# Kernel tuning notes

Hardware: AMD Instinct MI355X
Metric: run time of the kernel (lower is better)

The kernel has to match this reference:

```python
import jax, jax.numpy as jnp
import numpy as np

N_NODES = 50000
N_EDGES = 800000
N_GRAPHS = 64
EPS = 1e-5


def glorot(key, shape):
    fan_in, fan_out = shape[0], shape[1]
    lim = np.sqrt(6.0 / (fan_in + fan_out))
    return jax.random.uniform(key, shape, jnp.float32, -lim, lim)


def setup_inputs() -> dict:
    key = jax.random.key(0)
    ks = jax.random.split(key, 12)
    x = jax.random.normal(ks[0], (N_NODES, 1), jnp.float32)
    edge_index = jax.random.randint(ks[1], (2, N_EDGES), 0, N_NODES, jnp.int64)
    batch = jnp.sort(jax.random.randint(ks[2], (N_NODES,), 0, N_GRAPHS, jnp.int64))
    dims = [(1, 256), (256, 256), (256, 128)]
    params = {}
    for i, (di, do) in enumerate(dims):
        params[f"Wl{i}"] = glorot(ks[3 + 3 * i], (di, do))          # neighbor (lin_l) weight
        params[f"b{i}"] = jnp.zeros((do,), jnp.float32)              # lin_l bias
        params[f"Wr{i}"] = glorot(ks[4 + 3 * i], (di, do))           # root (lin_r) weight
    params["gamma"] = jnp.ones((128,), jnp.float32)
    params["beta"] = jnp.zeros((128,), jnp.float32)
    return {"x": x, "edge_index": edge_index, "batch": batch, **params}


def _sage_conv(x, src, dst, deg_inv, Wl, b, Wr):
    # mean-aggregate messages x[src] at dst, then lin_l(agg) + lin_r(x)
    agg = jax.ops.segment_sum(x[src], dst, num_segments=N_NODES) * deg_inv
    return agg @ Wl + b + x @ Wr


def reference(x, edge_index, batch, Wl0, b0, Wr0, Wl1, b1, Wr1, Wl2, b2, Wr2, gamma, beta):
    src, dst = edge_index[0], edge_index[1]
    deg = jax.ops.segment_sum(jnp.ones((N_EDGES,), x.dtype), dst, num_segments=N_NODES)
    deg_inv = (1.0 / jnp.maximum(deg, 1.0))[:, None]

    h = _sage_conv(x, src, dst, deg_inv, Wl0, b0, Wr0)
    h = jax.nn.relu(h)  # dropout is identity in eval mode
    h = _sage_conv(h, src, dst, deg_inv, Wl1, b1, Wr1)
    h = jax.nn.relu(h)
    h = _sage_conv(h, src, dst, deg_inv, Wl2, b2, Wr2)

    # global mean pool over graphs
    gsum = jax.ops.segment_sum(h, batch, num_segments=N_GRAPHS)
    gcnt = jax.ops.segment_sum(jnp.ones((N_NODES,), h.dtype), batch, num_segments=N_GRAPHS)
    g = gsum / jnp.maximum(gcnt, 1.0)[:, None]

    # LayerNorm over feature dim
    mu = jnp.mean(g, axis=-1, keepdims=True)
    var = jnp.var(g, axis=-1, keepdims=True)
    return (g - mu) * jax.lax.rsqrt(var + EPS) * gamma + beta
```

## Files before the change

kernel.cpp:

```cpp
#include <hip/hip_runtime.h>
#include <stdint.h>

#define NN 50000
#define NE 800000
#define NG 64
#define F1 256
#define NNP 50176
#define NBK 196
#define NBS 392
#define EPB 2048
#define SCB 391
#define PCHUNKS 112
#define PKC 448

typedef __bf16 bf16x8 __attribute__((ext_vector_type(8)));
typedef float f32x4 __attribute__((ext_vector_type(4)));

__device__ __forceinline__ float bf2f(unsigned int u) {
  union { float f; unsigned int i; } v; v.i = (u & 0xffffu) << 16; return v.f;
}
__device__ __forceinline__ unsigned short f2bf(float f) {
  union { float f; unsigned int i; } v; v.f = f;
  unsigned int r = v.i + 0x7fffu + ((v.i >> 16) & 1u);
  return (unsigned short)(r >> 16);
}
__device__ __forceinline__ float asf(unsigned int u) {
  union { unsigned int u; float f; } v; v.u = u; return v.f;
}
__device__ __forceinline__ unsigned int asu(float f) {
  union { float f; unsigned int u; } v; v.f = f; return v.u;
}

__global__ void k_bhist(const int* __restrict__ ei, int* __restrict__ btot_d,
                        int* __restrict__ btot_s) {
  __shared__ int lhd[NBK];
  __shared__ int lhs[NBS];
  for (int i = threadIdx.x; i < NBK; i += 256) lhd[i] = 0;
  for (int i = threadIdx.x; i < NBS; i += 256) lhs[i] = 0;
  __syncthreads();
  for (int e = blockIdx.x * blockDim.x + threadIdx.x; e < NE; e += gridDim.x * blockDim.x) {
    atomicAdd(&lhs[ei[e] >> 7], 1);
    atomicAdd(&lhd[ei[NE + e] >> 8], 1);
  }
  __syncthreads();
  for (int i = threadIdx.x; i < NBK; i += 256) atomicAdd(&btot_d[i], lhd[i]);
  for (int i = threadIdx.x; i < NBS; i += 256) atomicAdd(&btot_s[i], lhs[i]);
}

__global__ void k_bscan(const int* __restrict__ btot_d, const int* __restrict__ btot_s,
                        int* __restrict__ bbase, int* __restrict__ bcur,
                        int* __restrict__ sbase, int* __restrict__ scur,
                        int* __restrict__ rowp) {
  __shared__ int buf[512];
  int t = threadIdx.x;
  int v = (t < NBK) ? btot_d[t] : 0;
  buf[t] = v;
  __syncthreads();
  for (int off = 1; off < 512; off <<= 1) {
    int o = (t >= off) ? buf[t - off] : 0;
    __syncthreads();
    buf[t] += o;
    __syncthreads();
  }
  if (t < NBK) { bbase[t] = buf[t] - v; bcur[t] = buf[t] - v; }
  if (t == NBK - 1) bbase[NBK] = buf[t];
  __syncthreads();
  int v2 = (t < NBS) ? btot_s[t] : 0;
  buf[t] = v2;
  __syncthreads();
  for (int off = 1; off < 512; off <<= 1) {
    int o = (t >= off) ? buf[t - off] : 0;
    __syncthreads();
    buf[t] += o;
    __syncthreads();
  }
  if (t < NBS) { sbase[t] = buf[t] - v2; scur[t] = buf[t] - v2; }
  if (t == NBS - 1) sbase[NBS] = buf[t];
  if (t == 0) rowp[NN] = NE;
}

__global__ __launch_bounds__(256) void k_bscatter(
    const int* __restrict__ ei, const float* __restrict__ x,
    int* __restrict__ bcur, int* __restrict__ scur,
    uint2* __restrict__ recs, unsigned int* __restrict__ srecs) {
  __shared__ int lhd[NBK]; __shared__ int gbd[NBK];
  __shared__ int lhs[NBS]; __shared__ int gbs[NBS];
  int b = blockIdx.x, tid = threadIdx.x;
  int e0 = b * EPB;
  for (int i = tid; i < NBK; i += 256) lhd[i] = 0;
  for (int i = tid; i < NBS; i += 256) lhs[i] = 0;
  __syncthreads();
  unsigned int meta[8]; float xv[8]; int lofd[8]; int bkd[8]; int lofs[8]; int bks[8];
#pragma unroll
  for (int i = 0; i < 8; ++i) {
    int e = e0 + i * 256 + tid;
    bkd[i] = -1;
    if (e < NE) {
      int s = ei[e], d = ei[NE + e];
      bkd[i] = d >> 8; bks[i] = s >> 7;
      meta[i] = (unsigned int)s | ((unsigned int)d << 16);
      xv[i] = x[s];
      lofd[i] = atomicAdd(&lhd[bkd[i]], 1);
      lofs[i] = atomicAdd(&lhs[bks[i]], 1);
    }
  }
  __syncthreads();
  for (int i = tid; i < NBK; i += 256) gbd[i] = atomicAdd(&bcur[i], lhd[i]);
  for (int i = tid; i < NBS; i += 256) gbs[i] = atomicAdd(&scur[i], lhs[i]);
  __syncthreads();
#pragma unroll
  for (int i = 0; i < 8; ++i) {
    if (bkd[i] >= 0) {
      recs[gbd[bkd[i]] + lofd[i]] = make_uint2(meta[i], asu(xv[i]));
      unsigned int s = meta[i] & 0xFFFFu, d = meta[i] >> 16;
      srecs[gbs[bks[i]] + lofs[i]] = d | ((s & 127u) << 16);
    }
  }
}

__global__ __launch_bounds__(256) void k_csr(
    const uint2* __restrict__ recs, const int* __restrict__ bbase,
    const float* __restrict__ x, const int* __restrict__ batch,
    int* __restrict__ rowp, float2* __restrict__ ax,
    int* __restrict__ colx, uint2* __restrict__ dg) {
  __shared__ int cnt[256];
  __shared__ int sc[256];
  __shared__ float xs[256];
  int b = blockIdx.x, tid = threadIdx.x;
  int eb = bbase[b], ee = bbase[b + 1];
  cnt[tid] = 0;
  xs[tid] = 0.0f;
  __syncthreads();
  for (int e = eb + tid; e < ee; e += 256) {
    uint2 r = recs[e];
    int dl = (r.x >> 16) & 255;
    atomicAdd(&cnt[dl], 1);
    atomicAdd(&xs[dl], asf(r.y));
  }
  __syncthreads();
  sc[tid] = cnt[tid];
  __syncthreads();
  for (int off = 1; off < 256; off <<= 1) {
    int o = (tid >= off) ? sc[tid - off] : 0;
    __syncthreads();
    sc[tid] += o;
    __syncthreads();
  }
  int excl = sc[tid] - cnt[tid];
  int i = b * 256 + tid;
  float dinv = 1.0f / fmaxf((float)cnt[tid], 1.0f);
  if (i < NN) {
    rowp[i] = eb + excl;
    ax[i] = make_float2(xs[tid] * dinv, x[i]);
    dg[i] = make_uint2(asu(dinv), (unsigned int)batch[i]);
  }
  __syncthreads();
  sc[tid] = excl;
  __syncthreads();
  for (int e = eb + tid; e < ee; e += 256) {
    uint2 r = recs[e];
    int dl = (r.x >> 16) & 255;
    int s = r.x & 0xFFFF;
    int slot = atomicAdd(&sc[dl], 1);
    colx[eb + slot] = s;
  }
}

__global__ __launch_bounds__(256) void k_csc(
    const unsigned int* __restrict__ srecs, const int* __restrict__ sbase,
    const uint2* __restrict__ dg, unsigned int* __restrict__ wgT2u) {
  __shared__ float wgrow[128 * 65];
  int b = blockIdx.x, tid = threadIdx.x;
  for (int i = tid; i < 128 * 65; i += 256) wgrow[i] = 0.0f;
  __syncthreads();
  int eb = sbase[b], ee = sbase[b + 1];
  for (int e = eb + tid; e < ee; e += 256) {
    unsigned int r = srecs[e];
    int d = r & 0xFFFF;
    int sl = (r >> 16) & 127;
    uint2 t = dg[d];
    atomicAdd(&wgrow[sl * 65 + t.y], asf(t.x));
  }
  __syncthreads();
  int s0u = b * 64;
  int k = tid & 63;
  for (int rr = 0; rr < 16; ++rr) {
    int g = rr * 4 + (tid >> 6);
    float w0 = wgrow[(2 * k) * 65 + g];
    float w1 = wgrow[(2 * k + 1) * 65 + g];
    unsigned short h0 = f2bf(w0), h1v = f2bf(w1);
    unsigned short l0 = f2bf(w0 - bf2f(h0)), l1 = f2bf(w1 - bf2f(h1v));
    wgT2u[(size_t)g * (NNP / 2) + s0u + k] = (unsigned int)h0 | ((unsigned int)h1v << 16);
    wgT2u[(size_t)(64 + g) * (NNP / 2) + s0u + k] = (unsigned int)l0 | ((unsigned int)l1 << 16);
  }
}

__global__ void k_cnt(const int* __restrict__ batch, int* __restrict__ cnt) {
  int g = threadIdx.x;
  if (g >= NG) return;
  int lo = 0, hi = NN;
  while (lo < hi) { int m = (lo + hi) >> 1; if (batch[m] < g) lo = m + 1; else hi = m; }
  int a = lo;
  lo = 0; hi = NN;
  while (lo < hi) { int m = (lo + hi) >> 1; if (batch[m] < g + 1) lo = m + 1; else hi = m; }
  cnt[g] = lo - a;
}

__global__ void k_axe(const int* __restrict__ colx, const float2* __restrict__ ax,
                      float2* __restrict__ axe) {
  int e = blockIdx.x * blockDim.x + threadIdx.x;
  if (e >= NE) return;
  axe[e] = ax[colx[e]];
}

__global__ void k_wprep(const float* __restrict__ Wl1, const float* __restrict__ Wr1,
                        unsigned short* __restrict__ wcat) {
  int t = blockIdx.x * blockDim.x + threadIdx.x;
  if (t >= 256 * 512) return;
  int n = t >> 9, k = t & 511;
  float v = (k < 256) ? Wl1[k * 256 + n] : Wr1[(k - 256) * 256 + n];
  wcat[t] = f2bf(v);
}

__global__ __launch_bounds__(256) void k_agg2(
    const float2* __restrict__ axe, const int* __restrict__ rowp,
    const float* __restrict__ Wl0, const float* __restrict__ b0,
    const float* __restrict__ Wr0, unsigned short* __restrict__ aggb) {
  int wid = threadIdx.x >> 6, lane = threadIdx.x & 63;
  int gw = blockIdx.x * 4 + wid;
  int tw = gridDim.x * 4;
  float wl[4], wr[4], bb[4];
#pragma unroll
  for (int k = 0; k < 4; ++k) {
    wl[k] = Wl0[lane * 4 + k];
    wr[k] = Wr0[lane * 4 + k];
    bb[k] = b0[lane * 4 + k];
  }
  for (int d = gw; d < NN; d += tw) {
    int beg = rowp[d], end = rowp[d + 1];
    float a[4] = {0.f, 0.f, 0.f, 0.f};
    float c[4] = {0.f, 0.f, 0.f, 0.f};
    int e = beg;
    for (; e + 3 < end; e += 4) {
      float2 v0 = axe[e], v1 = axe[e + 1], v2 = axe[e + 2], v3 = axe[e + 3];
#pragma unroll
      for (int k = 0; k < 4; ++k) {
        a[k] += fmaxf(fmaf(v0.x, wl[k], fmaf(v0.y, wr[k], bb[k])), 0.0f);
        c[k] += fmaxf(fmaf(v1.x, wl[k], fmaf(v1.y, wr[k], bb[k])), 0.0f);
        a[k] += fmaxf(fmaf(v2.x, wl[k], fmaf(v2.y, wr[k], bb[k])), 0.0f);
        c[k] += fmaxf(fmaf(v3.x, wl[k], fmaf(v3.y, wr[k], bb[k])), 0.0f);
      }
    }
    for (; e < end; ++e) {
      float2 v0 = axe[e];
#pragma unroll
      for (int k = 0; k < 4; ++k)
        a[k] += fmaxf(fmaf(v0.x, wl[k], fmaf(v0.y, wr[k], bb[k])), 0.0f);
    }
    float dinv = 1.0f / fmaxf((float)(end - beg), 1.0f);
    uint2 o;
    o.x = (unsigned int)f2bf((a[0] + c[0]) * dinv) | ((unsigned int)f2bf((a[1] + c[1]) * dinv) << 16);
    o.y = (unsigned int)f2bf((a[2] + c[2]) * dinv) | ((unsigned int)f2bf((a[3] + c[3]) * dinv) << 16);
    *(uint2*)(aggb + (size_t)d * F1 + lane * 4) = o;
  }
}

#define BM 128
#define BN 128
#define BK 32

__global__ __launch_bounds__(256) void k_gemm1(
    const unsigned short* __restrict__ aggb, const float2* __restrict__ ax,
    const unsigned short* __restrict__ wcat,
    const float* __restrict__ Wl0, const float* __restrict__ b0,
    const float* __restrict__ Wr0, const float* __restrict__ b1,
    const int* __restrict__ batch, float* __restrict__ p1,
    unsigned short* __restrict__ h1T) {
  __shared__ unsigned char SMEM[35840];
  typedef unsigned short ush;
  ush (*As)[BM][BK] = (ush (*)[BM][BK])SMEM;
  ush (*Bs)[BN][BK] = (ush (*)[BN][BK])(SMEM + 16384);
  float* wl0s = (float*)(SMEM + 32768);
  float* wr0s = wl0s + 256;
  float* b0s = wl0s + 512;
  ush* Ts = (ush*)SMEM;

  int bm = blockIdx.x, ct = blockIdx.y;
  int tid = threadIdx.x;
  int wid = tid >> 6, lane = tid & 63;
  int wr = wid >> 1, wc = wid & 1;
  int rc = lane & 15, kh = lane >> 4;
  int r0 = bm * BM;
  int srow = tid >> 1;
  int sslot = tid & 1;

  wl0s[tid] = Wl0[tid];
  wr0s[tid] = Wr0[tid];
  b0s[tid] = b0[tid];

  int rA = r0 + srow;
  bool rAok = rA < NN;
  float2 axv = rAok ? ax[rA] : make_float2(0.f, 0.f);

  f32x4 acc[4][4] = {};
  int4 ra0, ra1, rb0, rb1;

#define LOAD_A(kt)                                                             \
  do {                                                                         \
    ra0 = make_int4(0, 0, 0, 0); ra1 = make_int4(0, 0, 0, 0);                  \
    if (rAok) {                                                                \
      const int4* s_ = (const int4*)(aggb + (size_t)rA * F1 + (kt) * BK + sslot * 16); \
      ra0 = s_[0]; ra1 = s_[1];                                                \
    }                                                                          \
  } while (0)

#define LOAD_B(kt)                                                             \
  do {                                                                         \
    const int4* t_ = (const int4*)(wcat + (size_t)(ct * BN + srow) * 512 + (kt) * BK + sslot * 16); \
    rb0 = t_[0]; rb1 = t_[1];                                                  \
  } while (0)

#define COMP_A(kt)                                                             \
  do {                                                                         \
    int j0_ = ((kt) - 8) * BK + sslot * 16;                                    \
    unsigned int w_[8];                                                        \
    _Pragma("unroll") for (int q = 0; q < 8; ++q) {                            \
      int j_ = j0_ + 2 * q;                                                    \
      float f0_ = fmaxf(fmaf(axv.x, wl0s[j_], fmaf(axv.y, wr0s[j_], b0s[j_])), 0.0f); \
      float f1_ = fmaxf(fmaf(axv.x, wl0s[j_ + 1], fmaf(axv.y, wr0s[j_ + 1], b0s[j_ + 1])), 0.0f); \
      w_[q] = (unsigned int)f2bf(f0_) | ((unsigned int)f2bf(f1_) << 16);       \
    }                                                                          \
    ra0 = make_int4(w_[0], w_[1], w_[2], w_[3]);                               \
    ra1 = make_int4(w_[4], w_[5], w_[6], w_[7]);                               \
  } while (0)

#define WRITE_AB(buf)                                                          \
  do {                                                                         \
    int sw_ = (srow >> 1) & 3;                                                 \
    int ws0_ = (2 * sslot) ^ sw_;                                              \
    int ws1_ = (2 * sslot + 1) ^ sw_;                                          \
    *(int4*)&As[buf][srow][ws0_ * 8] = ra0;                                    \
    *(int4*)&As[buf][srow][ws1_ * 8] = ra1;                                    \
    *(int4*)&Bs[buf][srow][ws0_ * 8] = rb0;                                    \
    *(int4*)&Bs[buf][srow][ws1_ * 8] = rb1;                                    \
  } while (0)

  LOAD_B(0);
  LOAD_A(0);
  WRITE_AB(0);
  __syncthreads();
  int cur = 0;
  for (int kt = 0; kt < 16; ++kt) {
    if (kt < 15) {
      LOAD_B(kt + 1);
      if (kt + 1 < 8) LOAD_A(kt + 1);
    }
    bf16x8 af[4], bfr[4];
#pragma unroll
    for (int mf = 0; mf < 4; ++mf) {
      int row = wr * 64 + mf * 16 + rc;
      int sl = kh ^ ((row >> 1) & 3);
      af[mf] = *(const bf16x8*)&As[cur][row][sl * 8];
    }
#pragma unroll
    for (int nf = 0; nf < 4; ++nf) {
      int row = wc * 64 + nf * 16 + rc;
      int sl = kh ^ ((row >> 1) & 3);
      bfr[nf] = *(const bf16x8*)&Bs[cur][row][sl * 8];
    }
#pragma unroll
    for (int nf = 0; nf < 4; ++nf)
#pragma unroll
      for (int mf = 0; mf < 4; ++mf)
        acc[nf][mf] = __builtin_amdgcn_mfma_f32_16x16x32_bf16(bfr[nf], af[mf], acc[nf][mf], 0, 0, 0);
    if (kt < 15) {
      if (kt + 1 >= 8) COMP_A(kt + 1);
      WRITE_AB(cur ^ 1);
    }
    __syncthreads();
    cur ^= 1;
  }
#undef LOAD_A
#undef LOAD_B
#undef COMP_A
#undef WRITE_AB

  int gv[4];
#pragma unroll
  for (int mf = 0; mf < 4; ++mf) {
    int s = r0 + wr * 64 + mf * 16 + rc;
    gv[mf] = (s < NN) ? batch[s] : -1;
  }
  int g0 = 0, g1 = -1;
  if (r0 < NN) {
    g0 = batch[r0];
    g1 = batch[min(r0 + 127, NN - 1)];
  }

#pragma unroll
  for (int nf = 0; nf < 4; ++nf) {
    int c0l = wc * 64 + nf * 16 + kh * 4;
    float4 bbq = *(const float4*)(b1 + ct * BN + c0l);
    float bbv[4] = {bbq.x, bbq.y, bbq.z, bbq.w};
    float v[4][4];
#pragma unroll
    for (int mf = 0; mf < 4; ++mf)
#pragma unroll
      for (int j = 0; j < 4; ++j)
        v[mf][j] = fmaxf(acc[nf][mf][j] + bbv[j], 0.0f);
#pragma unroll
    for (int mf = 0; mf < 4; ++mf) {
      int s_loc = wr * 64 + mf * 16 + rc;
#pragma unroll
      for (int j = 0; j < 4; ++j) {
        int f_loc = c0l + j;
        Ts[f_loc * 128 + (s_loc ^ ((f_loc & 7) << 3))] = f2bf(v[mf][j]);
      }
    }
    for (int g = g0; g <= g1; ++g) {
#pragma unroll
      for (int j = 0; j < 4; ++j) {
        float s = 0.f;
#pragma unroll
        for (int mf = 0; mf < 4; ++mf) s += (gv[mf] == g) ? v[mf][j] : 0.f;
        s += __shfl_xor(s, 1); s += __shfl_xor(s, 2);
        s += __shfl_xor(s, 4); s += __shfl_xor(s, 8);
        if (rc == 0 && s != 0.f) atomicAdd(&p1[g * F1 + ct * BN + c0l + j], s);
      }
    }
  }
  __syncthreads();
  {
    int f_loc = tid >> 1;
    int sh = (tid & 1) * 64;
    size_t rowoff = (size_t)(ct * BN + f_loc) * NNP + (size_t)bm * BM;
#pragma unroll
    for (int q = 0; q < 8; ++q) {
      int s_l = sh + q * 8;
      int4 vv = *(const int4*)&Ts[f_loc * 128 + (s_l ^ ((f_loc & 7) << 3))];
      *(int4*)(h1T + rowoff + s_l) = vv;
    }
  }
}

__global__ __launch_bounds__(512) void k_poolmm(
    const unsigned short* __restrict__ h1T, const unsigned short* __restrict__ wgT2,
    float* __restrict__ zpart) {
  int bid = blockIdx.x;
  int c = bid % PCHUNKS, fh = bid / PCHUNKS;
  int tid = threadIdx.x;
  int w = tid >> 6, lane = tid & 63, rc = lane & 15, kh = lane >> 4;
  size_t soff = (size_t)c * PKC + kh * 8;
  const unsigned short* bp = h1T + (size_t)(fh * 128 + w * 16 + rc) * NNP + soff;
  const unsigned short* ap = wgT2 + (size_t)rc * NNP + soff;
  f32x4 acc[8] = {};
  bf16x8 a0[8], a1[8], bA, bB;
#define PLOADS(da, db, ks)                                                     \
  do {                                                                         \
    db = *(const bf16x8*)(bp + (ks) * 32);                                     \
    _Pragma("unroll") for (int mt = 0; mt < 8; ++mt)                           \
      da[mt] = *(const bf16x8*)(ap + (size_t)mt * 16 * NNP + (ks) * 32);       \
  } while (0)
  PLOADS(a0, bA, 0);
  for (int ks = 0; ks < 14; ks += 2) {
    PLOADS(a1, bB, ks + 1);
#pragma unroll
    for (int mt = 0; mt < 8; ++mt)
      acc[mt] = __builtin_amdgcn_mfma_f32_16x16x32_bf16(a0[mt], bA, acc[mt], 0, 0, 0);
    if (ks + 2 < 14) PLOADS(a0, bA, ks + 2);
#pragma unroll
    for (int mt = 0; mt < 8; ++mt)
      acc[mt] = __builtin_amdgcn_mfma_f32_16x16x32_bf16(a1[mt], bB, acc[mt], 0, 0, 0);
  }
#undef PLOADS
  float* zp = zpart + ((size_t)c * 128) * F1 + fh * 128 + w * 16 + rc;
#pragma unroll
  for (int mt = 0; mt < 8; ++mt)
#pragma unroll
    for (int r = 0; r < 4; ++r)
      zp[(size_t)(mt * 16 + kh * 4 + r) * F1] = acc[mt][r];
}

__global__ void k_zred(const float* __restrict__ zpart, float* __restrict__ z) {
  int g = blockIdx.x, q = blockIdx.y, t = threadIdx.x;
  float a = 0.0f;
  for (int c = q * 28; c < q * 28 + 28; ++c)
    a += zpart[((size_t)c * 128 + g) * F1 + t] + zpart[((size_t)c * 128 + 64 + g) * F1 + t];
  atomicAdd(&z[g * F1 + t], a);
}

__global__ void k_final(const float* __restrict__ z, const float* __restrict__ p1,
                        const int* __restrict__ cnt,
                        const float* __restrict__ Wl2, const float* __restrict__ b2,
                        const float* __restrict__ Wr2, const float* __restrict__ gamma,
                        const float* __restrict__ beta, float* __restrict__ out) {
  __shared__ float s1[128], s2[128];
  int g = blockIdx.x, j = threadIdx.x;
  float invc = 1.0f / fmaxf((float)cnt[g], 1.0f);
  float acc = 0.0f;
  for (int k = 0; k < 256; ++k) {
    acc += z[g * 256 + k] * Wl2[k * 128 + j] + p1[g * 256 + k] * Wr2[k * 128 + j];
  }
  acc = acc * invc + b2[j];
  s1[j] = acc; s2[j] = acc * acc;
  __syncthreads();
  for (int off = 64; off > 0; off >>= 1) {
    if (j < off) { s1[j] += s1[j + off]; s2[j] += s2[j + off]; }
    __syncthreads();
  }
  float mu = s1[0] / 128.0f;
  float var = s2[0] / 128.0f - mu * mu;
  out[g * 128 + j] = (acc - mu) * rsqrtf(var + 1e-5f) * gamma[j] + beta[j];
}

extern "C" void kernel_launch(void* const* d_in, const int* in_sizes, int n_in,
                              void* d_out, int out_size, void* d_ws, size_t ws_size,
                              hipStream_t stream) {
  const float* x = (const float*)d_in[0];
  const int* ei = (const int*)d_in[1];
  const int* batch = (const int*)d_in[2];
  const float* Wl0 = (const float*)d_in[3];
  const float* b0 = (const float*)d_in[4];
  const float* Wr0 = (const float*)d_in[5];
  const float* Wl1 = (const float*)d_in[6];
  const float* b1 = (const float*)d_in[7];
  const float* Wr1 = (const float*)d_in[8];
  const float* Wl2 = (const float*)d_in[9];
  const float* b2 = (const float*)d_in[10];
  const float* Wr2 = (const float*)d_in[11];
  const float* gamma = (const float*)d_in[12];
  const float* beta = (const float*)d_in[13];
  float* out = (float*)d_out;

  char* p = (char*)d_ws;
  auto alloc = [&](size_t bytes) {
    char* r = p;
    p += (bytes + 511) & ~(size_t)511;
    return r;
  };
  unsigned short* h1T = (unsigned short*)alloc((size_t)F1 * NNP * 2);
  unsigned short* aggb = (unsigned short*)alloc((size_t)NN * F1 * 2);
  float2* axe = (float2*)alloc((size_t)NE * 8);
  int* rowp = (int*)alloc((size_t)(NN + 1) * 4);
  float2* ax = (float2*)alloc((size_t)NN * 8);
  uint2* dg = (uint2*)alloc((size_t)NN * 8);
  int* cnt = (int*)alloc((size_t)NG * 4);
  float* z = (float*)alloc((size_t)NG * F1 * 4);
  float* p1 = (float*)alloc((size_t)NG * F1 * 4);
  unsigned short* wcat = (unsigned short*)alloc((size_t)256 * 512 * 2);
  int* btot_d = (int*)alloc((size_t)NBK * 4);
  int* btot_s = (int*)alloc((size_t)NBS * 4);
  int* bbase = (int*)alloc((size_t)(NBK + 1) * 4);
  int* bcur = (int*)alloc((size_t)NBK * 4);
  int* sbase = (int*)alloc((size_t)(NBS + 1) * 4);
  int* scur = (int*)alloc((size_t)NBS * 4);
  unsigned short* wgT2 = (unsigned short*)alloc((size_t)128 * NNP * 2);
  uint2* recs = (uint2*)aggb;
  unsigned int* srecs = (unsigned int*)(aggb + (size_t)NE * 4);
  int* colx = (int*)(aggb + (size_t)NE * 6);
  float* zpart = (float*)aggb;

  hipMemsetAsync(btot_d, 0, (size_t)NBK * 4, stream);
  hipMemsetAsync(btot_s, 0, (size_t)NBS * 4, stream);
  hipMemsetAsync(p1, 0, (size_t)NG * F1 * 4, stream);
  hipMemsetAsync(z, 0, (size_t)NG * F1 * 4, stream);

  k_bhist<<<256, 256, 0, stream>>>(ei, btot_d, btot_s);
  k_bscan<<<1, 512, 0, stream>>>(btot_d, btot_s, bbase, bcur, sbase, scur, rowp);
  k_bscatter<<<SCB, 256, 0, stream>>>(ei, x, bcur, scur, recs, srecs);
  k_csr<<<NBK, 256, 0, stream>>>(recs, bbase, x, batch, rowp, ax, colx, dg);
  k_csc<<<NBS, 256, 0, stream>>>(srecs, sbase, dg, (unsigned int*)wgT2);
  k_cnt<<<1, 64, 0, stream>>>(batch, cnt);
  k_axe<<<(NE + 255) / 256, 256, 0, stream>>>(colx, ax, axe);
  k_wprep<<<(256 * 512 + 255) / 256, 256, 0, stream>>>(Wl1, Wr1, wcat);
  k_agg2<<<2048, 256, 0, stream>>>(axe, rowp, Wl0, b0, Wr0, aggb);
  dim3 gg(392, 2);
  k_gemm1<<<gg, 256, 0, stream>>>(aggb, ax, wcat, Wl0, b0, Wr0, b1, batch, p1, h1T);
  k_poolmm<<<2 * PCHUNKS, 512, 0, stream>>>(h1T, wgT2, zpart);
  dim3 zg(NG, 4);
  k_zred<<<zg, 256, 0, stream>>>(zpart, z);
  k_final<<<NG, 128, 0, stream>>>(z, p1, cnt, Wl2, b2, Wr2, gamma, beta, out);
}
```

Baseline: 223.2 us.

## Fold graph pooling of h1 into pool GEMM via one-hot rows; drop LDS staging in gemm1

The per-graph sum of h1 (p1) was computed in the gemm1 epilogue with shuffles and global atomics. It is now computed by adding 64 one-hot batch-membership rows to the pooling weight matrix, so k_poolmm produces p1 alongside z, and k_zred reduces both. gemm1 also drops its shared-memory double-buffered A/B tiles and loads MFMA fragments directly from global memory into registers, with launch bounds of 2 blocks per SM. The cost is 50% more MFMA work and A-matrix traffic in poolmm, extra zpart storage, and possibly less coalesced global loads in gemm1.

```diff
diff --git a/kernel.cpp b/kernel.cpp
--- a/kernel.cpp
+++ b/kernel.cpp
@@ -12,6 +12,7 @@
 #define SCB 391
 #define PCHUNKS 112
 #define PKC 448
+#define ZROWS 192
 
 typedef __bf16 bf16x8 __attribute__((ext_vector_type(8)));
 typedef float f32x4 __attribute__((ext_vector_type(4)));
@@ -168,10 +169,16 @@
 
 __global__ __launch_bounds__(256) void k_csc(
     const unsigned int* __restrict__ srecs, const int* __restrict__ sbase,
-    const uint2* __restrict__ dg, unsigned int* __restrict__ wgT2u) {
+    const uint2* __restrict__ dg, const int* __restrict__ batch,
+    unsigned int* __restrict__ wgT3u) {
   __shared__ float wgrow[128 * 65];
+  __shared__ int sbt[128];
   int b = blockIdx.x, tid = threadIdx.x;
   for (int i = tid; i < 128 * 65; i += 256) wgrow[i] = 0.0f;
+  if (tid < 128) {
+    int s = b * 128 + tid;
+    sbt[tid] = (s < NN) ? batch[s] : -1;
+  }
   __syncthreads();
   int eb = sbase[b], ee = sbase[b + 1];
   for (int e = eb + tid; e < ee; e += 256) {
@@ -190,8 +197,14 @@
     float w1 = wgrow[(2 * k + 1) * 65 + g];
     unsigned short h0 = f2bf(w0), h1v = f2bf(w1);
     unsigned short l0 = f2bf(w0 - bf2f(h0)), l1 = f2bf(w1 - bf2f(h1v));
-    wgT2u[(size_t)g * (NNP / 2) + s0u + k] = (unsigned int)h0 | ((unsigned int)h1v << 16);
-    wgT2u[(size_t)(64 + g) * (NNP / 2) + s0u + k] = (unsigned int)l0 | ((unsigned int)l1 << 16);
+    wgT3u[(size_t)g * (NNP / 2) + s0u + k] = (unsigned int)h0 | ((unsigned int)h1v << 16);
+    wgT3u[(size_t)(64 + g) * (NNP / 2) + s0u + k] = (unsigned int)l0 | ((unsigned int)l1 << 16);
+  }
+  int bv0 = sbt[2 * k], bv1 = sbt[2 * k + 1];
+  for (int rr = 0; rr < 16; ++rr) {
+    int g = rr * 4 + (tid >> 6);
+    unsigned int u = ((bv0 == g) ? 0x3F80u : 0u) | ((bv1 == g) ? 0x3F800000u : 0u);
+    wgT3u[(size_t)(128 + g) * (NNP / 2) + s0u + k] = u;
   }
 }
 
@@ -267,165 +280,106 @@
 
 #define BM 128
 #define BN 128
-#define BK 32
-
-__global__ __launch_bounds__(256) void k_gemm1(
+
+__global__ __launch_bounds__(256, 2) void k_gemm1(
     const unsigned short* __restrict__ aggb, const float2* __restrict__ ax,
     const unsigned short* __restrict__ wcat,
     const float* __restrict__ Wl0, const float* __restrict__ b0,
     const float* __restrict__ Wr0, const float* __restrict__ b1,
-    const int* __restrict__ batch, float* __restrict__ p1,
     unsigned short* __restrict__ h1T) {
-  __shared__ unsigned char SMEM[35840];
-  typedef unsigned short ush;
-  ush (*As)[BM][BK] = (ush (*)[BM][BK])SMEM;
-  ush (*Bs)[BN][BK] = (ush (*)[BN][BK])(SMEM + 16384);
-  float* wl0s = (float*)(SMEM + 32768);
-  float* wr0s = wl0s + 256;
-  float* b0s = wl0s + 512;
-  ush* Ts = (ush*)SMEM;
-
+  __shared__ float wl0s[256], wr0s[256], b0s[256];
+  __shared__ unsigned short Ts[128 * 128];
   int bm = blockIdx.x, ct = blockIdx.y;
   int tid = threadIdx.x;
   int wid = tid >> 6, lane = tid & 63;
   int wr = wid >> 1, wc = wid & 1;
   int rc = lane & 15, kh = lane >> 4;
   int r0 = bm * BM;
-  int srow = tid >> 1;
-  int sslot = tid & 1;
 
   wl0s[tid] = Wl0[tid];
   wr0s[tid] = Wr0[tid];
   b0s[tid] = b0[tid];
 
-  int rA = r0 + srow;
-  bool rAok = rA < NN;
-  float2 axv = rAok ? ax[rA] : make_float2(0.f, 0.f);
+  int arow[4]; bool aok[4]; float2 axr[4];
+#pragma unroll
+  for (int mf = 0; mf < 4; ++mf) {
+    arow[mf] = r0 + wr * 64 + mf * 16 + rc;
+    aok[mf] = arow[mf] < NN;
+    axr[mf] = aok[mf] ? ax[arow[mf]] : make_float2(0.f, 0.f);
+  }
+  __syncthreads();
+
+  const unsigned short* bp = wcat + (size_t)(ct * BN + wc * 64 + rc) * 512 + kh * 8;
 
   f32x4 acc[4][4] = {};
-  int4 ra0, ra1, rb0, rb1;
-
-#define LOAD_A(kt)                                                             \
+  bf16x8 af[2][4], bf[2][4];
+
+#define LOADB(buf, kt)                                                         \
   do {                                                                         \
-    ra0 = make_int4(0, 0, 0, 0); ra1 = make_int4(0, 0, 0, 0);                  \
-    if (rAok) {                                                                \
-      const int4* s_ = (const int4*)(aggb + (size_t)rA * F1 + (kt) * BK + sslot * 16); \
-      ra0 = s_[0]; ra1 = s_[1];                                                \
+    _Pragma("unroll") for (int nf = 0; nf < 4; ++nf)                           \
+      bf[buf][nf] = *(const bf16x8*)(bp + nf * 16 * 512 + (kt) * 32);          \
+  } while (0)
+
+#define LOADA(buf, kt)                                                         \
+  do {                                                                         \
+    _Pragma("unroll") for (int mf = 0; mf < 4; ++mf) {                         \
+      int4 t_ = make_int4(0, 0, 0, 0);                                         \
+      if (aok[mf]) t_ = *(const int4*)(aggb + (size_t)arow[mf] * F1 + (kt) * 32 + kh * 8); \
+      af[buf][mf] = *(const bf16x8*)&t_;                                       \
     }                                                                          \
   } while (0)
 
-#define LOAD_B(kt)                                                             \
+#define COMPA(buf, kt)                                                         \
   do {                                                                         \
-    const int4* t_ = (const int4*)(wcat + (size_t)(ct * BN + srow) * 512 + (kt) * BK + sslot * 16); \
-    rb0 = t_[0]; rb1 = t_[1];                                                  \
+    int f0_ = ((kt) - 8) * 32 + kh * 8;                                        \
+    float4 wla_ = *(const float4*)&wl0s[f0_], wlb_ = *(const float4*)&wl0s[f0_ + 4]; \
+    float4 wra_ = *(const float4*)&wr0s[f0_], wrb_ = *(const float4*)&wr0s[f0_ + 4]; \
+    float4 ba_ = *(const float4*)&b0s[f0_], bb_ = *(const float4*)&b0s[f0_ + 4]; \
+    float wlv_[8] = {wla_.x, wla_.y, wla_.z, wla_.w, wlb_.x, wlb_.y, wlb_.z, wlb_.w}; \
+    float wrv_[8] = {wra_.x, wra_.y, wra_.z, wra_.w, wrb_.x, wrb_.y, wrb_.z, wrb_.w}; \
+    float bbv_[8] = {ba_.x, ba_.y, ba_.z, ba_.w, bb_.x, bb_.y, bb_.z, bb_.w};  \
+    _Pragma("unroll") for (int mf = 0; mf < 4; ++mf) {                         \
+      bf16x8 h_;                                                               \
+      _Pragma("unroll") for (int q = 0; q < 8; ++q) {                          \
+        float v_ = fmaxf(fmaf(axr[mf].x, wlv_[q], fmaf(axr[mf].y, wrv_[q], bbv_[q])), 0.0f); \
+        h_[q] = (__bf16)v_;                                                    \
+      }                                                                        \
+      af[buf][mf] = h_;                                                        \
+    }                                                                          \
   } while (0)
 
-#define COMP_A(kt)                                                             \
-  do {                                                                         \
-    int j0_ = ((kt) - 8) * BK + sslot * 16;                                    \
-    unsigned int w_[8];                                                        \
-    _Pragma("unroll") for (int q = 0; q < 8; ++q) {                            \
-      int j_ = j0_ + 2 * q;                                                    \
-      float f0_ = fmaxf(fmaf(axv.x, wl0s[j_], fmaf(axv.y, wr0s[j_], b0s[j_])), 0.0f); \
-      float f1_ = fmaxf(fmaf(axv.x, wl0s[j_ + 1], fmaf(axv.y, wr0s[j_ + 1], b0s[j_ + 1])), 0.0f); \
-      w_[q] = (unsigned int)f2bf(f0_) | ((unsigned int)f2bf(f1_) << 16);       \
-    }                                                                          \
-    ra0 = make_int4(w_[0], w_[1], w_[2], w_[3]);                               \
-    ra1 = make_int4(w_[4], w_[5], w_[6], w_[7]);                               \
-  } while (0)
-
-#define WRITE_AB(buf)                                                          \
-  do {                                                                         \
-    int sw_ = (srow >> 1) & 3;                                                 \
-    int ws0_ = (2 * sslot) ^ sw_;                                              \
-    int ws1_ = (2 * sslot + 1) ^ sw_;                                          \
-    *(int4*)&As[buf][srow][ws0_ * 8] = ra0;                                    \
-    *(int4*)&As[buf][srow][ws1_ * 8] = ra1;                                    \
-    *(int4*)&Bs[buf][srow][ws0_ * 8] = rb0;                                    \
-    *(int4*)&Bs[buf][srow][ws1_ * 8] = rb1;                                    \
-  } while (0)
-
-  LOAD_B(0);
-  LOAD_A(0);
-  WRITE_AB(0);
-  __syncthreads();
-  int cur = 0;
+  LOADB(0, 0);
+  LOADA(0, 0);
+#pragma unroll
   for (int kt = 0; kt < 16; ++kt) {
+    int cb = kt & 1, nb = (kt + 1) & 1;
     if (kt < 15) {
-      LOAD_B(kt + 1);
-      if (kt + 1 < 8) LOAD_A(kt + 1);
-    }
-    bf16x8 af[4], bfr[4];
-#pragma unroll
-    for (int mf = 0; mf < 4; ++mf) {
-      int row = wr * 64 + mf * 16 + rc;
-      int sl = kh ^ ((row >> 1) & 3);
-      af[mf] = *(const bf16x8*)&As[cur][row][sl * 8];
-    }
-#pragma unroll
-    for (int nf = 0; nf < 4; ++nf) {
-      int row = wc * 64 + nf * 16 + rc;
-      int sl = kh ^ ((row >> 1) & 3);
-      bfr[nf] = *(const bf16x8*)&Bs[cur][row][sl * 8];
+      LOADB(nb, kt + 1);
+      if (kt + 1 < 8) LOADA(nb, kt + 1); else COMPA(nb, kt + 1);
     }
 #pragma unroll
     for (int nf = 0; nf < 4; ++nf)
 #pragma unroll
       for (int mf = 0; mf < 4; ++mf)
-        acc[nf][mf] = __builtin_amdgcn_mfma_f32_16x16x32_bf16(bfr[nf], af[mf], acc[nf][mf], 0, 0, 0);
-    if (kt < 15) {
-      if (kt + 1 >= 8) COMP_A(kt + 1);
-      WRITE_AB(cur ^ 1);
-    }
-    __syncthreads();
-    cur ^= 1;
-  }
-#undef LOAD_A
-#undef LOAD_B
-#undef COMP_A
-#undef WRITE_AB
-
-  int gv[4];
-#pragma unroll
-  for (int mf = 0; mf < 4; ++mf) {
-    int s = r0 + wr * 64 + mf * 16 + rc;
-    gv[mf] = (s < NN) ? batch[s] : -1;
-  }
-  int g0 = 0, g1 = -1;
-  if (r0 < NN) {
-    g0 = batch[r0];
-    g1 = batch[min(r0 + 127, NN - 1)];
-  }
+        acc[nf][mf] = __builtin_amdgcn_mfma_f32_16x16x32_bf16(bf[cb][nf], af[cb][mf], acc[nf][mf], 0, 0, 0);
+  }
+#undef LOADB
+#undef LOADA
+#undef COMPA
 
 #pragma unroll
   for (int nf = 0; nf < 4; ++nf) {
     int c0l = wc * 64 + nf * 16 + kh * 4;
     float4 bbq = *(const float4*)(b1 + ct * BN + c0l);
     float bbv[4] = {bbq.x, bbq.y, bbq.z, bbq.w};
-    float v[4][4];
-#pragma unroll
-    for (int mf = 0; mf < 4; ++mf)
-#pragma unroll
-      for (int j = 0; j < 4; ++j)
-        v[mf][j] = fmaxf(acc[nf][mf][j] + bbv[j], 0.0f);
 #pragma unroll
     for (int mf = 0; mf < 4; ++mf) {
       int s_loc = wr * 64 + mf * 16 + rc;
 #pragma unroll
       for (int j = 0; j < 4; ++j) {
+        float v = fmaxf(acc[nf][mf][j] + bbv[j], 0.0f);
         int f_loc = c0l + j;
-        Ts[f_loc * 128 + (s_loc ^ ((f_loc & 7) << 3))] = f2bf(v[mf][j]);
-      }
-    }
-    for (int g = g0; g <= g1; ++g) {
-#pragma unroll
-      for (int j = 0; j < 4; ++j) {
-        float s = 0.f;
-#pragma unroll
-        for (int mf = 0; mf < 4; ++mf) s += (gv[mf] == g) ? v[mf][j] : 0.f;
-        s += __shfl_xor(s, 1); s += __shfl_xor(s, 2);
-        s += __shfl_xor(s, 4); s += __shfl_xor(s, 8);
-        if (rc == 0 && s != 0.f) atomicAdd(&p1[g * F1 + ct * BN + c0l + j], s);
+        Ts[f_loc * 128 + (s_loc ^ ((f_loc & 7) << 3))] = f2bf(v);
       }
     }
   }
@@ -444,7 +398,7 @@
 }
 
 __global__ __launch_bounds__(512) void k_poolmm(
-    const unsigned short* __restrict__ h1T, const unsigned short* __restrict__ wgT2,
+    const unsigned short* __restrict__ h1T, const unsigned short* __restrict__ wgT3,
     float* __restrict__ zpart) {
   int bid = blockIdx.x;
   int c = bid % PCHUNKS, fh = bid / PCHUNKS;
@@ -452,41 +406,46 @@
   int w = tid >> 6, lane = tid & 63, rc = lane & 15, kh = lane >> 4;
   size_t soff = (size_t)c * PKC + kh * 8;
   const unsigned short* bp = h1T + (size_t)(fh * 128 + w * 16 + rc) * NNP + soff;
-  const unsigned short* ap = wgT2 + (size_t)rc * NNP + soff;
-  f32x4 acc[8] = {};
-  bf16x8 a0[8], a1[8], bA, bB;
+  const unsigned short* ap = wgT3 + (size_t)rc * NNP + soff;
+  f32x4 acc[12] = {};
+  bf16x8 a0[12], a1[12], bA, bB;
 #define PLOADS(da, db, ks)                                                     \
   do {                                                                         \
     db = *(const bf16x8*)(bp + (ks) * 32);                                     \
-    _Pragma("unroll") for (int mt = 0; mt < 8; ++mt)                           \
+    _Pragma("unroll") for (int mt = 0; mt < 12; ++mt)                          \
       da[mt] = *(const bf16x8*)(ap + (size_t)mt * 16 * NNP + (ks) * 32);       \
   } while (0)
   PLOADS(a0, bA, 0);
   for (int ks = 0; ks < 14; ks += 2) {
     PLOADS(a1, bB, ks + 1);
 #pragma unroll
-    for (int mt = 0; mt < 8; ++mt)
+    for (int mt = 0; mt < 12; ++mt)
       acc[mt] = __builtin_amdgcn_mfma_f32_16x16x32_bf16(a0[mt], bA, acc[mt], 0, 0, 0);
     if (ks + 2 < 14) PLOADS(a0, bA, ks + 2);
 #pragma unroll
-    for (int mt = 0; mt < 8; ++mt)
+    for (int mt = 0; mt < 12; ++mt)
       acc[mt] = __builtin_amdgcn_mfma_f32_16x16x32_bf16(a1[mt], bB, acc[mt], 0, 0, 0);
   }
 #undef PLOADS
-  float* zp = zpart + ((size_t)c * 128) * F1 + fh * 128 + w * 16 + rc;
-#pragma unroll
-  for (int mt = 0; mt < 8; ++mt)
+  float* zp = zpart + ((size_t)c * ZROWS) * F1 + fh * 128 + w * 16 + rc;
+#pragma unroll
+  for (int mt = 0; mt < 12; ++mt)
 #pragma unroll
     for (int r = 0; r < 4; ++r)
       zp[(size_t)(mt * 16 + kh * 4 + r) * F1] = acc[mt][r];
 }
 
-__global__ void k_zred(const float* __restrict__ zpart, float* __restrict__ z) {
+__global__ void k_zred(const float* __restrict__ zpart, float* __restrict__ z,
+                       float* __restrict__ p1) {
   int g = blockIdx.x, q = blockIdx.y, t = threadIdx.x;
-  float a = 0.0f;
-  for (int c = q * 28; c < q * 28 + 28; ++c)
-    a += zpart[((size_t)c * 128 + g) * F1 + t] + zpart[((size_t)c * 128 + 64 + g) * F1 + t];
+  float a = 0.0f, b = 0.0f;
+  for (int c = q * 28; c < q * 28 + 28; ++c) {
+    const float* base = zpart + (size_t)c * ZROWS * F1;
+    a += base[(size_t)g * F1 + t] + base[(size_t)(64 + g) * F1 + t];
+    b += base[(size_t)(128 + g) * F1 + t];
+  }
   atomicAdd(&z[g * F1 + t], a);
+  atomicAdd(&p1[g * F1 + t], b);
 }
 
 __global__ void k_final(const float* __restrict__ z, const float* __restrict__ p1,
@@ -554,7 +513,7 @@
   int* bcur = (int*)alloc((size_t)NBK * 4);
   int* sbase = (int*)alloc((size_t)(NBS + 1) * 4);
   int* scur = (int*)alloc((size_t)NBS * 4);
-  unsigned short* wgT2 = (unsigned short*)alloc((size_t)128 * NNP * 2);
+  unsigned short* wgT3 = (unsigned short*)alloc((size_t)ZROWS * NNP * 2);
   uint2* recs = (uint2*)aggb;
   unsigned int* srecs = (unsigned int*)(aggb + (size_t)NE * 4);
   int* colx = (int*)(aggb + (size_t)NE * 6);
@@ -569,15 +528,15 @@
   k_bscan<<<1, 512, 0, stream>>>(btot_d, btot_s, bbase, bcur, sbase, scur, rowp);
   k_bscatter<<<SCB, 256, 0, stream>>>(ei, x, bcur, scur, recs, srecs);
   k_csr<<<NBK, 256, 0, stream>>>(recs, bbase, x, batch, rowp, ax, colx, dg);
-  k_csc<<<NBS, 256, 0, stream>>>(srecs, sbase, dg, (unsigned int*)wgT2);
+  k_csc<<<NBS, 256, 0, stream>>>(srecs, sbase, dg, batch, (unsigned int*)wgT3);
   k_cnt<<<1, 64, 0, stream>>>(batch, cnt);
   k_axe<<<(NE + 255) / 256, 256, 0, stream>>>(colx, ax, axe);
   k_wprep<<<(256 * 512 + 255) / 256, 256, 0, stream>>>(Wl1, Wr1, wcat);
   k_agg2<<<2048, 256, 0, stream>>>(axe, rowp, Wl0, b0, Wr0, aggb);
   dim3 gg(392, 2);
-  k_gemm1<<<gg, 256, 0, stream>>>(aggb, ax, wcat, Wl0, b0, Wr0, b1, batch, p1, h1T);
-  k_poolmm<<<2 * PCHUNKS, 512, 0, stream>>>(h1T, wgT2, zpart);
+  k_gemm1<<<gg, 256, 0, stream>>>(aggb, ax, wcat, Wl0, b0, Wr0, b1, h1T);
+  k_poolmm<<<2 * PCHUNKS, 512, 0, stream>>>(h1T, wgT3, zpart);
   dim3 zg(NG, 4);
-  k_zred<<<zg, 256, 0, stream>>>(zpart, z);
+  k_zred<<<zg, 256, 0, stream>>>(zpart, z, p1);
   k_final<<<NG, 128, 0, stream>>>(z, p1, cnt, Wl2, b2, Wr2, gamma, beta, out);
 }
```

Measured after the change: 244.6 us. +9.6%, slower.

## Move per-graph h1 pooling from GEMM epilogue into pooling MFMA via one-hot rows

Applied to the files above, without the earlier changes.

The per-graph sum of h1 (p1) is no longer computed with shuffles and atomics in the gemm1 epilogue. Instead, k_csc writes 64 extra one-hot batch-membership rows into the weight matrix, and k_poolmm computes those sums as 64 more MFMA output rows, which k_zred then reduces into p1. The gemm1 epilogue also drops its LDS transpose and writes bf16 h1T directly from the accumulators with 8-byte stores. In exchange, poolmm reads and computes 50% more A rows and keeps more registers live, and the direct stores are narrower and less coalesced.

```diff
diff --git a/kernel.cpp b/kernel.cpp
--- a/kernel.cpp
+++ b/kernel.cpp
@@ -12,6 +12,7 @@
 #define SCB 391
 #define PCHUNKS 112
 #define PKC 448
+#define ZROWS 192
 
 typedef __bf16 bf16x8 __attribute__((ext_vector_type(8)));
 typedef float f32x4 __attribute__((ext_vector_type(4)));
@@ -168,10 +169,16 @@
 
 __global__ __launch_bounds__(256) void k_csc(
     const unsigned int* __restrict__ srecs, const int* __restrict__ sbase,
-    const uint2* __restrict__ dg, unsigned int* __restrict__ wgT2u) {
+    const uint2* __restrict__ dg, const int* __restrict__ batch,
+    unsigned int* __restrict__ wgT3u) {
   __shared__ float wgrow[128 * 65];
+  __shared__ int sbt[128];
   int b = blockIdx.x, tid = threadIdx.x;
   for (int i = tid; i < 128 * 65; i += 256) wgrow[i] = 0.0f;
+  if (tid < 128) {
+    int s = b * 128 + tid;
+    sbt[tid] = (s < NN) ? batch[s] : -1;
+  }
   __syncthreads();
   int eb = sbase[b], ee = sbase[b + 1];
   for (int e = eb + tid; e < ee; e += 256) {
@@ -190,8 +197,14 @@
     float w1 = wgrow[(2 * k + 1) * 65 + g];
     unsigned short h0 = f2bf(w0), h1v = f2bf(w1);
     unsigned short l0 = f2bf(w0 - bf2f(h0)), l1 = f2bf(w1 - bf2f(h1v));
-    wgT2u[(size_t)g * (NNP / 2) + s0u + k] = (unsigned int)h0 | ((unsigned int)h1v << 16);
-    wgT2u[(size_t)(64 + g) * (NNP / 2) + s0u + k] = (unsigned int)l0 | ((unsigned int)l1 << 16);
+    wgT3u[(size_t)g * (NNP / 2) + s0u + k] = (unsigned int)h0 | ((unsigned int)h1v << 16);
+    wgT3u[(size_t)(64 + g) * (NNP / 2) + s0u + k] = (unsigned int)l0 | ((unsigned int)l1 << 16);
+  }
+  int bv0 = sbt[2 * k], bv1 = sbt[2 * k + 1];
+  for (int rr = 0; rr < 16; ++rr) {
+    int g = rr * 4 + (tid >> 6);
+    unsigned int u = ((bv0 == g) ? 0x3F80u : 0u) | ((bv1 == g) ? 0x3F800000u : 0u);
+    wgT3u[(size_t)(128 + g) * (NNP / 2) + s0u + k] = u;
   }
 }
 
@@ -274,17 +287,10 @@
     const unsigned short* __restrict__ wcat,
     const float* __restrict__ Wl0, const float* __restrict__ b0,
     const float* __restrict__ Wr0, const float* __restrict__ b1,
-    const int* __restrict__ batch, float* __restrict__ p1,
     unsigned short* __restrict__ h1T) {
-  __shared__ unsigned char SMEM[35840];
-  typedef unsigned short ush;
-  ush (*As)[BM][BK] = (ush (*)[BM][BK])SMEM;
-  ush (*Bs)[BN][BK] = (ush (*)[BN][BK])(SMEM + 16384);
-  float* wl0s = (float*)(SMEM + 32768);
-  float* wr0s = wl0s + 256;
-  float* b0s = wl0s + 512;
-  ush* Ts = (ush*)SMEM;
-
+  __shared__ unsigned short As[2][BM][BK];
+  __shared__ unsigned short Bs[2][BN][BK];
+  __shared__ float wl0s[256], wr0s[256], b0s[256];
   int bm = blockIdx.x, ct = blockIdx.y;
   int tid = threadIdx.x;
   int wid = tid >> 6, lane = tid & 63;
@@ -369,10 +375,10 @@
       bfr[nf] = *(const bf16x8*)&Bs[cur][row][sl * 8];
     }
 #pragma unroll
-    for (int nf = 0; nf < 4; ++nf)
-#pragma unroll
-      for (int mf = 0; mf < 4; ++mf)
-        acc[nf][mf] = __builtin_amdgcn_mfma_f32_16x16x32_bf16(bfr[nf], af[mf], acc[nf][mf], 0, 0, 0);
+    for (int mf = 0; mf < 4; ++mf)
+#pragma unroll
+      for (int nf = 0; nf < 4; ++nf)
+        acc[mf][nf] = __builtin_amdgcn_mfma_f32_16x16x32_bf16(af[mf], bfr[nf], acc[mf][nf], 0, 0, 0);
     if (kt < 15) {
       if (kt + 1 >= 8) COMP_A(kt + 1);
       WRITE_AB(cur ^ 1);
@@ -385,66 +391,26 @@
 #undef COMP_A
 #undef WRITE_AB
 
-  int gv[4];
-#pragma unroll
-  for (int mf = 0; mf < 4; ++mf) {
-    int s = r0 + wr * 64 + mf * 16 + rc;
-    gv[mf] = (s < NN) ? batch[s] : -1;
-  }
-  int g0 = 0, g1 = -1;
-  if (r0 < NN) {
-    g0 = batch[r0];
-    g1 = batch[min(r0 + 127, NN - 1)];
-  }
-
 #pragma unroll
   for (int nf = 0; nf < 4; ++nf) {
-    int c0l = wc * 64 + nf * 16 + kh * 4;
-    float4 bbq = *(const float4*)(b1 + ct * BN + c0l);
-    float bbv[4] = {bbq.x, bbq.y, bbq.z, bbq.w};
-    float v[4][4];
-#pragma unroll
-    for (int mf = 0; mf < 4; ++mf)
-#pragma unroll
-      for (int j = 0; j < 4; ++j)
-        v[mf][j] = fmaxf(acc[nf][mf][j] + bbv[j], 0.0f);
+    int f = ct * BN + wc * 64 + nf * 16 + rc;
+    float bias = b1[f];
+    size_t frow = (size_t)f * NNP;
 #pragma unroll
     for (int mf = 0; mf < 4; ++mf) {
-      int s_loc = wr * 64 + mf * 16 + rc;
-#pragma unroll
-      for (int j = 0; j < 4; ++j) {
-        int f_loc = c0l + j;
-        Ts[f_loc * 128 + (s_loc ^ ((f_loc & 7) << 3))] = f2bf(v[mf][j]);
-      }
-    }
-    for (int g = g0; g <= g1; ++g) {
-#pragma unroll
-      for (int j = 0; j < 4; ++j) {
-        float s = 0.f;
-#pragma unroll
-        for (int mf = 0; mf < 4; ++mf) s += (gv[mf] == g) ? v[mf][j] : 0.f;
-        s += __shfl_xor(s, 1); s += __shfl_xor(s, 2);
-        s += __shfl_xor(s, 4); s += __shfl_xor(s, 8);
-        if (rc == 0 && s != 0.f) atomicAdd(&p1[g * F1 + ct * BN + c0l + j], s);
-      }
-    }
-  }
-  __syncthreads();
-  {
-    int f_loc = tid >> 1;
-    int sh = (tid & 1) * 64;
-    size_t rowoff = (size_t)(ct * BN + f_loc) * NNP + (size_t)bm * BM;
-#pragma unroll
-    for (int q = 0; q < 8; ++q) {
-      int s_l = sh + q * 8;
-      int4 vv = *(const int4*)&Ts[f_loc * 128 + (s_l ^ ((f_loc & 7) << 3))];
-      *(int4*)(h1T + rowoff + s_l) = vv;
+      int s0 = r0 + wr * 64 + mf * 16 + kh * 4;
+      f32x4 a = acc[mf][nf];
+      unsigned int lo = (unsigned int)f2bf(fmaxf(a[0] + bias, 0.0f)) |
+                        ((unsigned int)f2bf(fmaxf(a[1] + bias, 0.0f)) << 16);
+      unsigned int hi = (unsigned int)f2bf(fmaxf(a[2] + bias, 0.0f)) |
+                        ((unsigned int)f2bf(fmaxf(a[3] + bias, 0.0f)) << 16);
+      *(uint2*)(h1T + frow + s0) = make_uint2(lo, hi);
     }
   }
 }
 
 __global__ __launch_bounds__(512) void k_poolmm(
-    const unsigned short* __restrict__ h1T, const unsigned short* __restrict__ wgT2,
+    const unsigned short* __restrict__ h1T, const unsigned short* __restrict__ wgT3,
     float* __restrict__ zpart) {
   int bid = blockIdx.x;
   int c = bid % PCHUNKS, fh = bid / PCHUNKS;
@@ -452,41 +418,46 @@
   int w = tid >> 6, lane = tid & 63, rc = lane & 15, kh = lane >> 4;
   size_t soff = (size_t)c * PKC + kh * 8;
   const unsigned short* bp = h1T + (size_t)(fh * 128 + w * 16 + rc) * NNP + soff;
-  const unsigned short* ap = wgT2 + (size_t)rc * NNP + soff;
-  f32x4 acc[8] = {};
-  bf16x8 a0[8], a1[8], bA, bB;
+  const unsigned short* ap = wgT3 + (size_t)rc * NNP + soff;
+  f32x4 acc[12] = {};
+  bf16x8 a0[12], a1[12], bA, bB;
 #define PLOADS(da, db, ks)                                                     \
   do {                                                                         \
     db = *(const bf16x8*)(bp + (ks) * 32);                                     \
-    _Pragma("unroll") for (int mt = 0; mt < 8; ++mt)                           \
+    _Pragma("unroll") for (int mt = 0; mt < 12; ++mt)                          \
       da[mt] = *(const bf16x8*)(ap + (size_t)mt * 16 * NNP + (ks) * 32);       \
   } while (0)
   PLOADS(a0, bA, 0);
   for (int ks = 0; ks < 14; ks += 2) {
     PLOADS(a1, bB, ks + 1);
 #pragma unroll
-    for (int mt = 0; mt < 8; ++mt)
+    for (int mt = 0; mt < 12; ++mt)
       acc[mt] = __builtin_amdgcn_mfma_f32_16x16x32_bf16(a0[mt], bA, acc[mt], 0, 0, 0);
     if (ks + 2 < 14) PLOADS(a0, bA, ks + 2);
 #pragma unroll
-    for (int mt = 0; mt < 8; ++mt)
+    for (int mt = 0; mt < 12; ++mt)
       acc[mt] = __builtin_amdgcn_mfma_f32_16x16x32_bf16(a1[mt], bB, acc[mt], 0, 0, 0);
   }
 #undef PLOADS
-  float* zp = zpart + ((size_t)c * 128) * F1 + fh * 128 + w * 16 + rc;
-#pragma unroll
-  for (int mt = 0; mt < 8; ++mt)
+  float* zp = zpart + ((size_t)c * ZROWS) * F1 + fh * 128 + w * 16 + rc;
+#pragma unroll
+  for (int mt = 0; mt < 12; ++mt)
 #pragma unroll
     for (int r = 0; r < 4; ++r)
       zp[(size_t)(mt * 16 + kh * 4 + r) * F1] = acc[mt][r];
 }
 
-__global__ void k_zred(const float* __restrict__ zpart, float* __restrict__ z) {
+__global__ void k_zred(const float* __restrict__ zpart, float* __restrict__ z,
+                       float* __restrict__ p1) {
   int g = blockIdx.x, q = blockIdx.y, t = threadIdx.x;
-  float a = 0.0f;
-  for (int c = q * 28; c < q * 28 + 28; ++c)
-    a += zpart[((size_t)c * 128 + g) * F1 + t] + zpart[((size_t)c * 128 + 64 + g) * F1 + t];
+  float a = 0.0f, b = 0.0f;
+  for (int c = q * 28; c < q * 28 + 28; ++c) {
+    const float* base = zpart + (size_t)c * ZROWS * F1;
+    a += base[(size_t)g * F1 + t] + base[(size_t)(64 + g) * F1 + t];
+    b += base[(size_t)(128 + g) * F1 + t];
+  }
   atomicAdd(&z[g * F1 + t], a);
+  atomicAdd(&p1[g * F1 + t], b);
 }
 
 __global__ void k_final(const float* __restrict__ z, const float* __restrict__ p1,
@@ -554,7 +525,7 @@
   int* bcur = (int*)alloc((size_t)NBK * 4);
   int* sbase = (int*)alloc((size_t)(NBS + 1) * 4);
   int* scur = (int*)alloc((size_t)NBS * 4);
-  unsigned short* wgT2 = (unsigned short*)alloc((size_t)128 * NNP * 2);
+  unsigned short* wgT3 = (unsigned short*)alloc((size_t)ZROWS * NNP * 2);
   uint2* recs = (uint2*)aggb;
   unsigned int* srecs = (unsigned int*)(aggb + (size_t)NE * 4);
   int* colx = (int*)(aggb + (size_t)NE * 6);
@@ -569,15 +540,15 @@
   k_bscan<<<1, 512, 0, stream>>>(btot_d, btot_s, bbase, bcur, sbase, scur, rowp);
   k_bscatter<<<SCB, 256, 0, stream>>>(ei, x, bcur, scur, recs, srecs);
   k_csr<<<NBK, 256, 0, stream>>>(recs, bbase, x, batch, rowp, ax, colx, dg);
-  k_csc<<<NBS, 256, 0, stream>>>(srecs, sbase, dg, (unsigned int*)wgT2);
+  k_csc<<<NBS, 256, 0, stream>>>(srecs, sbase, dg, batch, (unsigned int*)wgT3);
   k_cnt<<<1, 64, 0, stream>>>(batch, cnt);
   k_axe<<<(NE + 255) / 256, 256, 0, stream>>>(colx, ax, axe);
   k_wprep<<<(256 * 512 + 255) / 256, 256, 0, stream>>>(Wl1, Wr1, wcat);
   k_agg2<<<2048, 256, 0, stream>>>(axe, rowp, Wl0, b0, Wr0, aggb);
   dim3 gg(392, 2);
-  k_gemm1<<<gg, 256, 0, stream>>>(aggb, ax, wcat, Wl0, b0, Wr0, b1, batch, p1, h1T);
-  k_poolmm<<<2 * PCHUNKS, 512, 0, stream>>>(h1T, wgT2, zpart);
+  k_gemm1<<<gg, 256, 0, stream>>>(aggb, ax, wcat, Wl0, b0, Wr0, b1, h1T);
+  k_poolmm<<<2 * PCHUNKS, 512, 0, stream>>>(h1T, wgT3, zpart);
   dim3 zg(NG, 4);
-  k_zred<<<zg, 256, 0, stream>>>(zpart, z);
+  k_zred<<<zg, 256, 0, stream>>>(zpart, z, p1);
   k_final<<<NG, 128, 0, stream>>>(z, p1, cnt, Wl2, b2, Wr2, gamma, beta, out);
 }
```

Result: no change. 222.4 us (-0.4%).
